# Optimization experiments

Hardware: AMD Instinct MI355X
Metric: run time of the kernel (lower is better)

## Reference

```python
import jax, jax.numpy as jnp
import numpy as np

CONF_TH = 0.25   # default conf_thresh in non_max_suppression
NMS_TH = 0.35    # default nms_thresh


def setup_inputs() -> dict:
    key = jax.random.key(0)
    # [N, C=5+num_classes, H, W]
    preds = jax.random.normal(key, (64, 85, 32, 32), dtype=jnp.float32)
    return {"preds": preds}


def _decode(preds):
    """Faithful box decode: [N,C,H,W] -> [N, H*W, 6] (x1,y1,x2,y2,score,cls)."""
    N, C, H, W = preds.shape
    p = jnp.transpose(preds, (0, 2, 3, 1))           # [N,H,W,C]
    pobj = p[..., 0]
    preg = p[..., 1:5]
    pcls = p[..., 5:]
    score = pobj * jnp.max(pcls, axis=-1)             # obj * max-class
    cls = jax.lax.stop_gradient(jnp.argmax(pcls, axis=-1).astype(preds.dtype))
    gy, gx = jnp.meshgrid(jnp.arange(H, dtype=preds.dtype),
                          jnp.arange(W, dtype=preds.dtype), indexing="ij")
    bw = jax.nn.sigmoid(preg[..., 2])
    bh = jax.nn.sigmoid(preg[..., 3])
    bcx = (jnp.tanh(preg[..., 0]) + gx) / W
    bcy = (jnp.tanh(preg[..., 1]) + gy) / H
    x1 = bcx - 0.5 * bw
    y1 = bcy - 0.5 * bh
    x2 = bcx + 0.5 * bw
    y2 = bcy + 0.5 * bh
    bboxes = jnp.stack([x1, y1, x2, y2, score, cls], axis=-1)  # [N,H,W,6]
    return bboxes.reshape(N, H * W, 6)


def _iou_matrix(boxes):
    """[M,4] xyxy -> [M,M] pairwise IoU."""
    x1, y1, x2, y2 = boxes[:, 0], boxes[:, 1], boxes[:, 2], boxes[:, 3]
    area = (x2 - x1) * (y2 - y1)
    iw = jnp.clip(jnp.minimum(x2[:, None], x2[None, :]) - jnp.maximum(x1[:, None], x1[None, :]), 0.0)
    ih = jnp.clip(jnp.minimum(y2[:, None], y2[None, :]) - jnp.maximum(y1[:, None], y1[None, :]), 0.0)
    inter = iw * ih
    return inter / (area[:, None] + area[None, :] - inter + 1e-9)


def _nms_single(bb):
    """Greedy class-aware NMS on one image's [M,6] boxes.
    Equivalent to: filter score>CONF_TH then torchvision.batched_nms.
    Returns keep mask [M] in the original box order (fixed shape)."""
    M = bb.shape[0]
    order = jnp.argsort(-bb[:, 4])                    # descending score
    b = bb[order]
    iou = _iou_matrix(b[:, :4])
    same_cls = b[:, 5][:, None] == b[:, 5][None, :]
    supp_mat = (iou > NMS_TH) & same_cls              # [M,M]
    valid_s = b[:, 4] > CONF_TH

    def body(i, keep):
        suppressed = jnp.any(keep & supp_mat[i])
        return keep.at[i].set(valid_s[i] & ~suppressed)

    keep_s = jax.lax.fori_loop(0, M, body, jnp.zeros((M,), jnp.bool_))
    # scatter back to original order
    return jnp.zeros((M,), jnp.bool_).at[order].set(keep_s)


def reference(preds):
    bboxes = _decode(preds)                # [N, HW, 6]
    keep = jax.vmap(_nms_single)(bboxes)   # [N, HW] bool keep mask
    return bboxes, keep
```

## Files before the change

kernel.cpp:

```cpp
#include <hip/hip_runtime.h>
#include <math.h>

#define NIMG 64
#define HW   1024
#define NCH  85
#define NCLS 80
#define CONF_TH 0.25f
#define NMS_TH  0.35f

__device__ __forceinline__ float fast_tanh(float x) {
  float e = __expf(2.0f * x);
  return 1.0f - 2.0f * __builtin_amdgcn_rcpf(e + 1.0f);
}
__device__ __forceinline__ float fast_sigmoid(float x) {
  return __builtin_amdgcn_rcpf(1.0f + __expf(-x));
}

__global__ __launch_bounds__(1024) void fused_kernel(const float* __restrict__ preds,
                                                     float* __restrict__ out,
                                                     float* __restrict__ keepOut) {
  int n = blockIdx.x;
  int t = threadIdx.x;

  __shared__ float sx1[HW], sy1[HW], sx2[HW], sy2[HW], sarea[HW], sscore[HW];
  __shared__ int scls[HW];
  __shared__ int bucket[HW];
  __shared__ int sorted[HW];
  __shared__ int srank[HW];
  __shared__ unsigned long long supp[HW];
  __shared__ int cnt[NCLS], offs[NCLS], start[NCLS];

  if (t < NCLS) cnt[t] = 0;

  const float* base = preds + (size_t)n * (NCH * HW) + t;

  float pobj = base[0];
  float tx = base[1 * HW], ty = base[2 * HW];
  float tw = base[3 * HW], th = base[4 * HW];

  float b0 = base[5 * HW], b1 = base[6 * HW], b2 = base[7 * HW], b3 = base[8 * HW];
  int i0 = 0, i1 = 1, i2 = 2, i3 = 3;
#pragma unroll
  for (int c = 4; c < NCLS; c += 4) {
    float v0 = base[(5 + c) * HW];
    float v1 = base[(6 + c) * HW];
    float v2 = base[(7 + c) * HW];
    float v3 = base[(8 + c) * HW];
    if (v0 > b0) { b0 = v0; i0 = c; }
    if (v1 > b1) { b1 = v1; i1 = c + 1; }
    if (v2 > b2) { b2 = v2; i2 = c + 2; }
    if (v3 > b3) { b3 = v3; i3 = c + 3; }
  }
  float best = b0; int bc = i0;
  if (b1 > best || (b1 == best && i1 < bc)) { best = b1; bc = i1; }
  if (b2 > best || (b2 == best && i2 < bc)) { best = b2; bc = i2; }
  if (b3 > best || (b3 == best && i3 < bc)) { best = b3; bc = i3; }

  float score = pobj * best;

  float gx = (float)(t & 31);
  float gy = (float)(t >> 5);
  float bcx = (fast_tanh(tx) + gx) * 0.03125f;
  float bcy = (fast_tanh(ty) + gy) * 0.03125f;
  float bw = fast_sigmoid(tw);
  float bh = fast_sigmoid(th);

  float x1 = bcx - 0.5f * bw, y1 = bcy - 0.5f * bh;
  float x2 = bcx + 0.5f * bw, y2 = bcy + 0.5f * bh;

  size_t gb = (size_t)n * HW + t;
  float2* ob = (float2*)(out + gb * 6);
  ob[0] = make_float2(x1, y1);
  ob[1] = make_float2(x2, y2);
  ob[2] = make_float2(score, (float)bc);

  sx1[t] = x1; sy1[t] = y1; sx2[t] = x2; sy2[t] = y2;
  sarea[t] = (x2 - x1) * (y2 - y1);
  sscore[t] = score;
  scls[t] = bc;
  bool valid = score > CONF_TH;
  __syncthreads();

  keepOut[gb] = 0.0f;
  if (valid) atomicAdd(&cnt[bc], 1);
  __syncthreads();

  if (t < 64) {
    int c0 = (2 * t < NCLS) ? cnt[2 * t] : 0;
    int c1 = (2 * t + 1 < NCLS) ? cnt[2 * t + 1] : 0;
    int ps = c0 + c1;
    int x = ps;
#pragma unroll
    for (int d = 1; d < 64; d <<= 1) {
      int y = __shfl_up(x, d, 64);
      if (t >= d) x += y;
    }
    int excl = x - ps;
    if (2 * t < NCLS)     { start[2 * t] = excl;          offs[2 * t] = excl; }
    if (2 * t + 1 < NCLS) { start[2 * t + 1] = excl + c0; offs[2 * t + 1] = excl + c0; }
  }
  __syncthreads();

  if (valid) {
    int p = atomicAdd(&offs[bc], 1);
    bucket[p] = t;
  }
  __syncthreads();

  if (valid) {
    int s0 = start[bc], m = cnt[bc];
    int r = 0;
    for (int j = 0; j < m; ++j) {
      int jb = bucket[s0 + j];
      float sj = sscore[jb];
      r += (sj > score) || (sj == score && jb < t);
    }
    srank[t] = r;
    sorted[s0 + r] = t;
  }
  __syncthreads();

  if (valid) {
    int s0 = start[bc];
    int a = srank[t];
    int lim = a < 64 ? a : 64;
    unsigned long long mask = 0ull;
    for (int b = 0; b < lim; ++b) {
      int jb = sorted[s0 + b];
      float iw = fminf(x2, sx2[jb]) - fmaxf(x1, sx1[jb]);
      float ih = fminf(y2, sy2[jb]) - fmaxf(y1, sy1[jb]);
      iw = fmaxf(iw, 0.0f);
      ih = fmaxf(ih, 0.0f);
      float inter = iw * ih;
      float aar = (x2 - x1) * (y2 - y1);
      float iou = inter / (aar + sarea[jb] - inter + 1e-9f);
      if (iou > NMS_TH) mask |= (1ull << b);
    }
    supp[s0 + a] = mask;
  }
  __syncthreads();

  if (t < NCLS) {
    int m = cnt[t], s0 = start[t];
    if (m <= 64) {
      unsigned long long kept = 0ull;
      for (int a = 0; a < m; ++a) {
        unsigned long long sa = supp[s0 + a];
        if ((sa & kept) == 0ull) {
          kept |= (1ull << a);
          keepOut[(size_t)n * HW + sorted[s0 + a]] = 1.0f;
        }
      }
    } else {
      for (int a = 0; a < m; ++a) {
        int ia = sorted[s0 + a];
        float ax1 = sx1[ia], ay1 = sy1[ia], ax2 = sx2[ia], ay2 = sy2[ia];
        float aar = sarea[ia];
        bool kp = true;
        for (int b = 0; b < a; ++b) {
          if (!bucket[s0 + b]) continue;
          int jb = sorted[s0 + b];
          float iw = fminf(ax2, sx2[jb]) - fmaxf(ax1, sx1[jb]);
          float ih = fminf(ay2, sy2[jb]) - fmaxf(ay1, sy1[jb]);
          iw = fmaxf(iw, 0.0f);
          ih = fmaxf(ih, 0.0f);
          float inter = iw * ih;
          float iou = inter / (aar + sarea[jb] - inter + 1e-9f);
          if (iou > NMS_TH) { kp = false; break; }
        }
        bucket[s0 + a] = kp ? 1 : 0;
        if (kp) keepOut[(size_t)n * HW + ia] = 1.0f;
      }
    }
  }
}

extern "C" void kernel_launch(void* const* d_in, const int* in_sizes, int n_in,
                              void* d_out, int out_size, void* d_ws, size_t ws_size,
                              hipStream_t stream) {
  const float* preds = (const float*)d_in[0];
  float* out = (float*)d_out;
  float* keepOut = out + (size_t)NIMG * HW * 6;

  fused_kernel<<<NIMG, HW, 0, stream>>>(preds, out, keepOut);
}
```

Measured before the change: 82.07 us.

## Split class argmax across thread quarters with float4 vector loads

Each thread now handles four adjacent pixels over a quarter of the class channels using float4 loads, with partial max/argmax exchanged through shared memory and merged per pixel. Objectness and regression channels are staged via shared memory by the first quarter. This aims to cut load instruction count and per-thread serial latency in the decode phase, at the cost of much more LDS use and an extra barrier. The box area is also hoisted out of the IoU loop.

```diff
diff --git a/kernel.cpp b/kernel.cpp
--- a/kernel.cpp
+++ b/kernel.cpp
@@ -16,11 +16,32 @@
   return __builtin_amdgcn_rcpf(1.0f + __expf(-x));
 }
 
+template <int CL0, int NC>
+__device__ __forceinline__ void quarter_argmax(const float* __restrict__ bp,
+                                               float4& mv, int4& mi) {
+  float4 v = *(const float4*)(bp + (size_t)CL0 * HW);
+  float b0 = v.x, b1 = v.y, b2 = v.z, b3 = v.w;
+  int i0 = CL0 - 5, i1 = i0, i2 = i0, i3 = i0;
+#pragma unroll
+  for (int c = 1; c < NC; ++c) {
+    float4 u = *(const float4*)(bp + (size_t)(CL0 + c) * HW);
+    int ci = CL0 - 5 + c;
+    if (u.x > b0) { b0 = u.x; i0 = ci; }
+    if (u.y > b1) { b1 = u.y; i1 = ci; }
+    if (u.z > b2) { b2 = u.z; i2 = ci; }
+    if (u.w > b3) { b3 = u.w; i3 = ci; }
+  }
+  mv = make_float4(b0, b1, b2, b3);
+  mi = make_int4(i0, i1, i2, i3);
+}
+
 __global__ __launch_bounds__(1024) void fused_kernel(const float* __restrict__ preds,
                                                      float* __restrict__ out,
                                                      float* __restrict__ keepOut) {
   int n = blockIdx.x;
   int t = threadIdx.x;
+  int q  = t >> 8;
+  int pg = t & 255;
 
   __shared__ float sx1[HW], sy1[HW], sx2[HW], sy2[HW], sarea[HW], sscore[HW];
   __shared__ int scls[HW];
@@ -29,33 +50,43 @@
   __shared__ int srank[HW];
   __shared__ unsigned long long supp[HW];
   __shared__ int cnt[NCLS], offs[NCLS], start[NCLS];
+  __shared__ float pmaxv[4][HW];
+  __shared__ int   pmaxi[4][HW];
+  __shared__ float sobj[HW];
+  __shared__ float sreg[4][HW];
 
   if (t < NCLS) cnt[t] = 0;
 
-  const float* base = preds + (size_t)n * (NCH * HW) + t;
-
-  float pobj = base[0];
-  float tx = base[1 * HW], ty = base[2 * HW];
-  float tw = base[3 * HW], th = base[4 * HW];
-
-  float b0 = base[5 * HW], b1 = base[6 * HW], b2 = base[7 * HW], b3 = base[8 * HW];
-  int i0 = 0, i1 = 1, i2 = 2, i3 = 3;
-#pragma unroll
-  for (int c = 4; c < NCLS; c += 4) {
-    float v0 = base[(5 + c) * HW];
-    float v1 = base[(6 + c) * HW];
-    float v2 = base[(7 + c) * HW];
-    float v3 = base[(8 + c) * HW];
-    if (v0 > b0) { b0 = v0; i0 = c; }
-    if (v1 > b1) { b1 = v1; i1 = c + 1; }
-    if (v2 > b2) { b2 = v2; i2 = c + 2; }
-    if (v3 > b3) { b3 = v3; i3 = c + 3; }
-  }
-  float best = b0; int bc = i0;
-  if (b1 > best || (b1 == best && i1 < bc)) { best = b1; bc = i1; }
-  if (b2 > best || (b2 == best && i2 < bc)) { best = b2; bc = i2; }
-  if (b3 > best || (b3 == best && i3 < bc)) { best = b3; bc = i3; }
-
+  const float* bp = preds + (size_t)n * (NCH * HW) + 4 * pg;
+  float4 mv; int4 mi;
+  if (q == 0) {
+    float4 vobj = *(const float4*)(bp);
+    ((float4*)sobj)[pg] = vobj;
+#pragma unroll
+    for (int r = 0; r < 4; ++r) {
+      float4 vr = *(const float4*)(bp + (size_t)(1 + r) * HW);
+      ((float4*)&sreg[r][0])[pg] = vr;
+    }
+    quarter_argmax<5, 16>(bp, mv, mi);
+  } else if (q == 1) {
+    quarter_argmax<21, 21>(bp, mv, mi);
+  } else if (q == 2) {
+    quarter_argmax<42, 21>(bp, mv, mi);
+  } else {
+    quarter_argmax<63, 22>(bp, mv, mi);
+  }
+  ((float4*)&pmaxv[q][0])[pg] = mv;
+  ((int4*)&pmaxi[q][0])[pg] = mi;
+  __syncthreads();
+
+  float pobj = sobj[t];
+  float tx = sreg[0][t], ty = sreg[1][t], tw = sreg[2][t], th = sreg[3][t];
+  float best = pmaxv[0][t]; int bc = pmaxi[0][t];
+#pragma unroll
+  for (int qq = 1; qq < 4; ++qq) {
+    float v = pmaxv[qq][t];
+    if (v > best) { best = v; bc = pmaxi[qq][t]; }
+  }
   float score = pobj * best;
 
   float gx = (float)(t & 31);
@@ -75,13 +106,14 @@
   ob[2] = make_float2(score, (float)bc);
 
   sx1[t] = x1; sy1[t] = y1; sx2[t] = x2; sy2[t] = y2;
-  sarea[t] = (x2 - x1) * (y2 - y1);
+  float aar = (x2 - x1) * (y2 - y1);
+  sarea[t] = aar;
   sscore[t] = score;
   scls[t] = bc;
   bool valid = score > CONF_TH;
-  __syncthreads();
-
   keepOut[gb] = 0.0f;
+  __syncthreads();
+
   if (valid) atomicAdd(&cnt[bc], 1);
   __syncthreads();
 
@@ -132,7 +164,6 @@
       iw = fmaxf(iw, 0.0f);
       ih = fmaxf(ih, 0.0f);
       float inter = iw * ih;
-      float aar = (x2 - x1) * (y2 - y1);
       float iou = inter / (aar + sarea[jb] - inter + 1e-9f);
       if (iou > NMS_TH) mask |= (1ull << b);
     }
@@ -155,7 +186,7 @@
       for (int a = 0; a < m; ++a) {
         int ia = sorted[s0 + a];
         float ax1 = sx1[ia], ay1 = sy1[ia], ax2 = sx2[ia], ay2 = sy2[ia];
-        float aar = sarea[ia];
+        float ar2 = sarea[ia];
         bool kp = true;
         for (int b = 0; b < a; ++b) {
           if (!bucket[s0 + b]) continue;
@@ -165,7 +196,7 @@
           iw = fmaxf(iw, 0.0f);
           ih = fmaxf(ih, 0.0f);
           float inter = iw * ih;
-          float iou = inter / (aar + sarea[jb] - inter + 1e-9f);
+          float iou = inter / (ar2 + sarea[jb] - inter + 1e-9f);
           if (iou > NMS_TH) { kp = false; break; }
         }
         bucket[s0 + a] = kp ? 1 : 0;
```

After: 73.31 us. 1.12x faster.
